# Kernel tuning notes

Hardware: AMD Instinct MI355X
Metric: run time of the kernel (lower is better)

The kernel has to match this reference:

```python
import jax, jax.numpy as jnp
import numpy as np

N_WORDS, MAX_W_LEN = 8192, 20
B, S = 64, 256
CH_SIZE, CH_EM, H = 128, 64, 256
W_SIZE, W_EM = 100000, 300
CAP_N, CAP_EM = 5, 16


def setup_inputs() -> dict:
    key = jax.random.key(0)
    ks = jax.random.split(key, 20)
    inp = {
        "ch": jax.random.randint(ks[0], (N_WORDS, MAX_W_LEN), 0, CH_SIZE),
        "rev_ch": jax.random.randint(ks[1], (N_WORDS, MAX_W_LEN), 0, CH_SIZE),
        "w_len": jax.random.randint(ks[2], (N_WORDS,), 1, MAX_W_LEN + 1),
        "w": jax.random.randint(ks[3], (B, S), 0, W_SIZE),
        "w_cap": jax.random.randint(ks[4], (B, S), 0, CAP_N),
        "w_chs": jax.random.randint(ks[5], (B, S), 0, N_WORDS),
        "w_mask": (jax.random.uniform(ks[6], (B, S)) > 0.1).astype(jnp.float32),
        "ch_em": jax.random.normal(ks[7], (CH_SIZE, CH_EM), jnp.float32) * 0.1,
        "w_em": jax.random.normal(ks[8], (W_SIZE, W_EM), jnp.float32) * 0.1,
        "cap_em": jax.random.normal(ks[9], (CAP_N, CAP_EM), jnp.float32) * 0.1,
        "fw_w_ih": jax.random.normal(ks[10], (3 * H, CH_EM), jnp.float32) * 0.05,
        "fw_w_hh": jax.random.normal(ks[11], (3 * H, H), jnp.float32) * 0.05,
        "fw_b_ih": jnp.zeros((3 * H,), jnp.float32),
        "fw_b_hh": jnp.zeros((3 * H,), jnp.float32),
        "bw_w_ih": jax.random.normal(ks[12], (3 * H, CH_EM), jnp.float32) * 0.05,
        "bw_w_hh": jax.random.normal(ks[13], (3 * H, H), jnp.float32) * 0.05,
        "bw_b_ih": jnp.zeros((3 * H,), jnp.float32),
        "bw_b_hh": jnp.zeros((3 * H,), jnp.float32),
    }
    return inp


def _gru_scan(x_seq, w_ih, w_hh, b_ih, b_hh, h0):
    """x_seq: [L, N, E]; returns stacked hidden states [L, N, H]. torch.nn.GRUCell math."""
    def step(h, x):
        gi = x @ w_ih.T + b_ih          # [N, 3H]
        gh = h @ w_hh.T + b_hh          # [N, 3H]
        i_r, i_z, i_n = jnp.split(gi, 3, axis=-1)
        h_r, h_z, h_n = jnp.split(gh, 3, axis=-1)
        r = jax.nn.sigmoid(i_r + h_r)
        z = jax.nn.sigmoid(i_z + h_z)
        n = jnp.tanh(i_n + r * h_n)
        h_new = (1.0 - z) * n + z * h
        return h_new, h_new
    _, hs = jax.lax.scan(step, h0, x_seq)
    return hs


def reference(ch, rev_ch, w_len, w, w_cap, w_chs, w_mask,
              ch_em, w_em, cap_em,
              fw_w_ih, fw_w_hh, fw_b_ih, fw_b_hh,
              bw_w_ih, bw_w_hh, bw_b_ih, bw_b_hh):
    n_words = ch.shape[0]
    h0 = jnp.zeros((n_words, H), ch_em.dtype)
    l_idx = (w_len - 1)[:, None, None]  # [N,1,1]

    # forward char RNN -> suffix states at last valid char
    fw_x = ch_em[ch].transpose(1, 0, 2)           # [L, N, E]
    fw_h = _gru_scan(fw_x, fw_w_ih, fw_w_hh, fw_b_ih, fw_b_hh, h0).transpose(1, 0, 2)  # [N, L, H]
    suffix_ems = jnp.take_along_axis(fw_h, l_idx, axis=1)[:, 0, :]  # [N, H]
    Suffixes = suffix_ems[w_chs]                  # [B, S, H]

    # backward char RNN (on reversed chars) -> prefix states
    bw_x = ch_em[rev_ch].transpose(1, 0, 2)
    bw_h = _gru_scan(bw_x, bw_w_ih, bw_w_hh, bw_b_ih, bw_b_hh, h0).transpose(1, 0, 2)
    prefix_ems = jnp.take_along_axis(bw_h, l_idx, axis=1)[:, 0, :]
    Prefixes = prefix_ems[w_chs]                  # [B, S, H]

    mask = w_mask[:, :, None]
    Words = w_em[w]                               # [B, S, W_EM]
    Caps = cap_em[w_cap]                          # [B, S, CAP_EM]
    features = jnp.concatenate(
        (Prefixes * mask, Words, Suffixes * mask, Caps), axis=2)
    return features
```

## Files before the change

kernel.cpp:

```cpp
#include <hip/hip_runtime.h>

#define NW    8192
#define MAXW  20
#define BB    64
#define SS    256
#define CHS   128
#define CHE   64
#define HH    256
#define G3    768
#define WEM   300
#define CAPEM 16

typedef _Float16 half8  __attribute__((ext_vector_type(8)));
typedef _Float16 half4v __attribute__((ext_vector_type(4)));
typedef float    f32x4  __attribute__((ext_vector_type(4)));

#define WF_OFF  0
#define GI_OFF  (2*G3*HH*2)
#define EMS_OFF (GI_OFF + 2*CHS*G3*2)

__device__ __forceinline__ float fast_sigmoid(float x) {
    float e = __builtin_amdgcn_exp2f(-1.442695041f * x);
    return __builtin_amdgcn_rcpf(1.0f + e);
}
__device__ __forceinline__ float fast_tanh(float x) {
    float e = __builtin_amdgcn_exp2f(2.885390082f * x);
    return 1.0f - 2.0f * __builtin_amdgcn_rcpf(1.0f + e);
}

__global__ void prep_w(const float* __restrict__ fw_whh, const float* __restrict__ bw_whh,
                       _Float16* __restrict__ Wf) {
    int dir = blockIdx.x / 48;
    int tile = blockIdx.x % 48;
    int g = tile >> 4, wvv = tile & 15;
    int t = threadIdx.x;
    int kk = t >> 6;
    int l16 = (t >> 2) & 15;
    int q = t & 3;
    int m = g * 256 + wvv * 16 + l16;
    const float* src = (dir ? bw_whh : fw_whh) + m * HH + kk * 32 + q * 8;
    _Float16* d = Wf + (size_t)dir * G3 * HH
                + (size_t)wvv * 12288 + g * 4096 + kk * 512 + (l16 * 4 + q) * 8;
    #pragma unroll
    for (int j = 0; j < 8; ++j) d[j] = (_Float16)src[j];
}

__global__ void prep_gi(const float* __restrict__ ch_em,
                        const float* __restrict__ fw_wih, const float* __restrict__ fw_bih,
                        const float* __restrict__ fw_bhh,
                        const float* __restrict__ bw_wih, const float* __restrict__ bw_bih,
                        const float* __restrict__ bw_bhh,
                        _Float16* __restrict__ gi) {
    int bx = blockIdx.x;
    int dir = bx >> 7;
    int c = bx & 127;
    const float* wih = dir ? bw_wih : fw_wih;
    const float* bih = dir ? bw_bih : fw_bih;
    const float* bhh = dir ? bw_bhh : fw_bhh;
    const float* ce = ch_em + c * CHE;
    for (int jj = 0; jj < 3; ++jj) {
        int j = jj * 256 + threadIdx.x;
        float s = bih[j] + (j < 512 ? bhh[j] : 0.0f);
        const float* wr = wih + j * CHE;
        #pragma unroll
        for (int e = 0; e < CHE; ++e) s += wr[e] * ce[e];
        gi[(size_t)dir * CHS * G3 + c * G3 + j] = (_Float16)s;
    }
}

__global__ __launch_bounds__(1024, 4)
void gru(const int* __restrict__ ch, const int* __restrict__ rev_ch,
         const int* __restrict__ wlen,
         const float* __restrict__ fw_bhh, const float* __restrict__ bw_bhh,
         const _Float16* __restrict__ Wf, const _Float16* __restrict__ gi,
         float* __restrict__ ems) {
    int dir = blockIdx.x >> 7;
    int wblk = blockIdx.x & 127;
    int w0 = wblk * 64;
    const int* chp = dir ? rev_ch : ch;
    const _Float16* W = Wf + (size_t)dir * G3 * HH;
    const _Float16* gt = gi + (size_t)dir * CHS * G3;
    const float* bh = dir ? bw_bhh : fw_bhh;
    float* emsd = ems + (size_t)dir * NW * HH;

    int tid = threadIdx.x;
    int wv = tid >> 6;
    int lane = tid & 63;
    int q = lane >> 4;
    int l16 = lane & 15;

    const _Float16* Wme = W + (size_t)wv * 12288 + (l16 * 4 + q) * 8;

    __shared__ __align__(16) _Float16 hbuf[64][264];
    __shared__ __align__(16) float    hbuf32[64][264];
    __shared__ int clds[64][MAXW];
    __shared__ int wls[64];

    for (int i = tid; i < 64 * 264; i += 1024) {
        (&hbuf[0][0])[i] = (_Float16)0.0f;
        (&hbuf32[0][0])[i] = 0.0f;
    }
    if (tid < 64) wls[tid] = wlen[w0 + tid];
    for (int i = tid; i < 64 * MAXW; i += 1024) {
        int w = i / MAXW, t = i - w * MAXW;
        clds[w][t] = chp[(w0 + w) * MAXW + t];
    }
    f32x4 bhhn = *(const f32x4*)(bh + 512 + wv * 16 + q * 4);
    const f32x4 fz = {0.0f, 0.0f, 0.0f, 0.0f};
    __syncthreads();

    #pragma unroll 1
    for (int t = 0; t < MAXW; ++t) {
        f32x4 acc[3][4];
        #pragma unroll
        for (int g = 0; g < 3; ++g)
            #pragma unroll
            for (int ct = 0; ct < 4; ++ct) acc[g][ct] = fz;

        #pragma unroll
        for (int kk = 0; kk < 8; ++kk) {
            half8 af0 = *(const half8*)(Wme + kk * 512);
            half8 af1 = *(const half8*)(Wme + 4096 + kk * 512);
            half8 af2 = *(const half8*)(Wme + 8192 + kk * 512);
            #pragma unroll
            for (int ct = 0; ct < 4; ++ct) {
                half8 bf = *(const half8*)(&hbuf[ct * 16 + l16][kk * 32 + q * 8]);
                acc[0][ct] = __builtin_amdgcn_mfma_f32_16x16x32_f16(af0, bf, acc[0][ct], 0, 0, 0);
                acc[1][ct] = __builtin_amdgcn_mfma_f32_16x16x32_f16(af1, bf, acc[1][ct], 0, 0, 0);
                acc[2][ct] = __builtin_amdgcn_mfma_f32_16x16x32_f16(af2, bf, acc[2][ct], 0, 0, 0);
            }
        }

        __syncthreads();

        #pragma unroll
        for (int ct = 0; ct < 4; ++ct) {
            int word = ct * 16 + l16;
            int c = clds[word][t];
            const _Float16* gr = gt + (size_t)c * G3 + wv * 16 + q * 4;
            half4v g0 = *(const half4v*)(gr);
            half4v g1 = *(const half4v*)(gr + 256);
            half4v g2 = *(const half4v*)(gr + 512);
            f32x4 hv = *(const f32x4*)(&hbuf32[word][wv * 16 + q * 4]);
            f32x4 out4;
            half4v hh4;
            #pragma unroll
            for (int e = 0; e < 4; ++e) {
                float r  = fast_sigmoid(acc[0][ct][e] + (float)g0[e]);
                float z  = fast_sigmoid(acc[1][ct][e] + (float)g1[e]);
                float n  = fast_tanh((float)g2[e] + r * (acc[2][ct][e] + bhhn[e]));
                float hnew = n + z * (hv[e] - n);
                out4[e] = hnew;
                hh4[e] = (_Float16)hnew;
            }
            *(half4v*)(&hbuf[word][wv * 16 + q * 4]) = hh4;
            *(f32x4*)(&hbuf32[word][wv * 16 + q * 4]) = out4;
        }
        __syncthreads();

        {
            int w = tid >> 4, t16 = tid & 15;
            if (wls[w] == t + 1) {
                const _Float16* src = &hbuf[w][t16 * 16];
                half8 a = *(const half8*)(src);
                half8 b = *(const half8*)(src + 8);
                f32x4 o0, o1, o2, o3;
                #pragma unroll
                for (int e = 0; e < 4; ++e) {
                    o0[e] = (float)a[e];     o1[e] = (float)a[4 + e];
                    o2[e] = (float)b[e];     o3[e] = (float)b[4 + e];
                }
                f32x4* dst = (f32x4*)(emsd + (size_t)(w0 + w) * HH + t16 * 16);
                dst[0] = o0; dst[1] = o1; dst[2] = o2; dst[3] = o3;
            }
        }
    }
}

__global__ void emit(const int* __restrict__ w, const int* __restrict__ wcap,
                     const int* __restrict__ wchs, const float* __restrict__ wmask,
                     const float* __restrict__ w_em, const float* __restrict__ cap_em,
                     const float* __restrict__ ems, float* __restrict__ out) {
    int pos = blockIdx.x;
    int c = threadIdx.x;
    if (c >= 207) return;
    int wi = w[pos], cap = wcap[pos], wch = wchs[pos];
    float m = wmask[pos];
    const f32x4* suf = (const f32x4*)(ems + (size_t)wch * HH);
    const f32x4* pre = (const f32x4*)(ems + (size_t)NW * HH + (size_t)wch * HH);
    const f32x4* wem = (const f32x4*)(w_em + (size_t)wi * WEM);
    const f32x4* cp4 = (const f32x4*)(cap_em + cap * CAPEM);
    f32x4 v;
    if (c < 64)       v = pre[c] * m;
    else if (c < 139) v = wem[c - 64];
    else if (c < 203) v = suf[c - 139] * m;
    else              v = cp4[c - 203];
    ((f32x4*)out)[(size_t)pos * 207 + c] = v;
}

extern "C" void kernel_launch(void* const* d_in, const int* in_sizes, int n_in,
                              void* d_out, int out_size, void* d_ws, size_t ws_size,
                              hipStream_t stream) {
    const int*   ch      = (const int*)d_in[0];
    const int*   rev_ch  = (const int*)d_in[1];
    const int*   w_len   = (const int*)d_in[2];
    const int*   w       = (const int*)d_in[3];
    const int*   w_cap   = (const int*)d_in[4];
    const int*   w_chs   = (const int*)d_in[5];
    const float* w_mask  = (const float*)d_in[6];
    const float* ch_em   = (const float*)d_in[7];
    const float* w_em    = (const float*)d_in[8];
    const float* cap_em  = (const float*)d_in[9];
    const float* fw_wih  = (const float*)d_in[10];
    const float* fw_whh  = (const float*)d_in[11];
    const float* fw_bih  = (const float*)d_in[12];
    const float* fw_bhh  = (const float*)d_in[13];
    const float* bw_wih  = (const float*)d_in[14];
    const float* bw_whh  = (const float*)d_in[15];
    const float* bw_bih  = (const float*)d_in[16];
    const float* bw_bhh  = (const float*)d_in[17];

    char* ws = (char*)d_ws;
    _Float16* Wf = (_Float16*)(ws + WF_OFF);
    _Float16* gi = (_Float16*)(ws + GI_OFF);
    float* ems   = (float*)(ws + EMS_OFF);
    float* out   = (float*)d_out;

    prep_w <<<96, 512, 0, stream>>>(fw_whh, bw_whh, Wf);
    prep_gi<<<256, 256, 0, stream>>>(ch_em, fw_wih, fw_bih, fw_bhh,
                                     bw_wih, bw_bih, bw_bhh, gi);
    gru    <<<256, 1024, 0, stream>>>(ch, rev_ch, w_len, fw_bhh, bw_bhh, Wf, gi, ems);
    emit   <<<BB * SS, 256, 0, stream>>>(w, w_cap, w_chs, w_mask, w_em, cap_em, ems, out);
}
```

Before: 511.7 us.

## Prefetch gate inputs to LDS asynchronously and keep fp32 hidden state in registers

```diff
diff --git a/kernel.cpp b/kernel.cpp
--- a/kernel.cpp
+++ b/kernel.cpp
@@ -26,6 +26,13 @@
 __device__ __forceinline__ float fast_tanh(float x) {
     float e = __builtin_amdgcn_exp2f(2.885390082f * x);
     return 1.0f - 2.0f * __builtin_amdgcn_rcpf(1.0f + e);
+}
+
+__device__ __forceinline__ void gl_lds16(const void* g, void* l) {
+    __builtin_amdgcn_global_load_lds(
+        (const __attribute__((address_space(1))) void*)g,
+        (__attribute__((address_space(3))) void*)l,
+        16, 0, 0);
 }
 
 __global__ void prep_w(const float* __restrict__ fw_whh, const float* __restrict__ bw_whh,
@@ -92,14 +99,11 @@
     const _Float16* Wme = W + (size_t)wv * 12288 + (l16 * 4 + q) * 8;
 
     __shared__ __align__(16) _Float16 hbuf[64][264];
-    __shared__ __align__(16) float    hbuf32[64][264];
+    __shared__ __align__(16) _Float16 gilds[96][64][8];
     __shared__ int clds[64][MAXW];
     __shared__ int wls[64];
 
-    for (int i = tid; i < 64 * 264; i += 1024) {
-        (&hbuf[0][0])[i] = (_Float16)0.0f;
-        (&hbuf32[0][0])[i] = 0.0f;
-    }
+    for (int i = tid; i < 64 * 264; i += 1024) (&hbuf[0][0])[i] = (_Float16)0.0f;
     if (tid < 64) wls[tid] = wlen[w0 + tid];
     for (int i = tid; i < 64 * MAXW; i += 1024) {
         int w = i / MAXW, t = i - w * MAXW;
@@ -107,10 +111,20 @@
     }
     f32x4 bhhn = *(const f32x4*)(bh + 512 + wv * 16 + q * 4);
     const f32x4 fz = {0.0f, 0.0f, 0.0f, 0.0f};
+    f32x4 hprev[4] = {fz, fz, fz, fz};
     __syncthreads();
 
     #pragma unroll 1
     for (int t = 0; t < MAXW; ++t) {
+        #pragma unroll
+        for (int it = 0; it < 6; ++it) {
+            int chunk = it * 1024 + tid;
+            int cch = chunk >> 6;
+            int word = chunk & 63;
+            int c = clds[word][t];
+            gl_lds16(gt + (size_t)c * G3 + cch * 8, &gilds[cch][word][0]);
+        }
+
         f32x4 acc[3][4];
         #pragma unroll
         for (int g = 0; g < 3; ++g)
@@ -133,28 +147,29 @@
 
         __syncthreads();
 
-        #pragma unroll
-        for (int ct = 0; ct < 4; ++ct) {
-            int word = ct * 16 + l16;
-            int c = clds[word][t];
-            const _Float16* gr = gt + (size_t)c * G3 + wv * 16 + q * 4;
-            half4v g0 = *(const half4v*)(gr);
-            half4v g1 = *(const half4v*)(gr + 256);
-            half4v g2 = *(const half4v*)(gr + 512);
-            f32x4 hv = *(const f32x4*)(&hbuf32[word][wv * 16 + q * 4]);
-            f32x4 out4;
-            half4v hh4;
+        {
+            int q2 = q >> 1, qo = (q & 1) * 4;
             #pragma unroll
-            for (int e = 0; e < 4; ++e) {
-                float r  = fast_sigmoid(acc[0][ct][e] + (float)g0[e]);
-                float z  = fast_sigmoid(acc[1][ct][e] + (float)g1[e]);
-                float n  = fast_tanh((float)g2[e] + r * (acc[2][ct][e] + bhhn[e]));
-                float hnew = n + z * (hv[e] - n);
-                out4[e] = hnew;
-                hh4[e] = (_Float16)hnew;
+            for (int ct = 0; ct < 4; ++ct) {
+                int word = ct * 16 + l16;
+                half4v g0 = *(const half4v*)(&gilds[wv * 2 + q2][word][qo]);
+                half4v g1 = *(const half4v*)(&gilds[wv * 2 + 32 + q2][word][qo]);
+                half4v g2 = *(const half4v*)(&gilds[wv * 2 + 64 + q2][word][qo]);
+                f32x4 hv = hprev[ct];
+                f32x4 out4;
+                half4v hh4;
+                #pragma unroll
+                for (int e = 0; e < 4; ++e) {
+                    float r  = fast_sigmoid(acc[0][ct][e] + (float)g0[e]);
+                    float z  = fast_sigmoid(acc[1][ct][e] + (float)g1[e]);
+                    float n  = fast_tanh((float)g2[e] + r * (acc[2][ct][e] + bhhn[e]));
+                    float hnew = n + z * (hv[e] - n);
+                    out4[e] = hnew;
+                    hh4[e] = (_Float16)hnew;
+                }
+                hprev[ct] = out4;
+                *(half4v*)(&hbuf[word][wv * 16 + q * 4]) = hh4;
             }
-            *(half4v*)(&hbuf[word][wv * 16 + q * 4]) = hh4;
-            *(f32x4*)(&hbuf32[word][wv * 16 + q * 4]) = out4;
         }
         __syncthreads();
 
```

Result: slower. 608.5 us (+18.9%).
